# Kernel optimization log

Hardware: AMD Instinct MI355X
Metric: run time of the kernel (lower is better)

## Reference

```python
import jax, jax.numpy as jnp
import numpy as np

K = 3            # TAGConv default number of hops
NUM_GRAPHS = 128 # graphs in the batch (for global_add_pool)


def _gcn_norm(src, dst, n):
    # PyG gcn_norm (symmetric, no self-loops): w_e = d[src]^-1/2 * d[dst]^-1/2
    deg = jnp.zeros((n,), jnp.float32).at[dst].add(1.0)
    dinv = jnp.where(deg > 0, jax.lax.rsqrt(deg), 0.0)
    return dinv[src] * dinv[dst]


def _tagconv(x, src, dst, wn, W, b):
    # out = sum_{k=0..K} (norm_adj^k x) @ W[k] + b
    n = x.shape[0]
    h = x
    out = h @ W[0]
    for k in range(1, K + 1):
        h = jax.ops.segment_sum(h[src] * wn[:, None], dst, num_segments=n)
        out = out + h @ W[k]
    return out + b


def setup_inputs() -> dict:
    key = jax.random.key(0)
    ks = jax.random.split(key, 8)
    N, E, D, H = 50000, 800000, 64, 64
    x = jax.random.normal(ks[0], (N, D), jnp.float32)
    edge_index = jax.random.randint(ks[1], (2, E), 0, N, dtype=jnp.int32)
    batch_ids = jnp.sort(jax.random.randint(ks[2], (N,), 0, NUM_GRAPHS, dtype=jnp.int32))
    def glorot(k, sh):
        return jax.random.normal(k, sh, jnp.float32) / np.float32(np.sqrt(sh[-2]))
    W0 = glorot(ks[3], (K + 1, D, H)); b0 = jnp.zeros((H,), jnp.float32)
    W1 = glorot(ks[4], (K + 1, H, H)); b1 = jnp.zeros((H,), jnp.float32)
    alpha0 = jnp.full((1,), 0.25, jnp.float32)  # PReLU default init
    alpha1 = jnp.full((1,), 0.25, jnp.float32)
    Wout = glorot(ks[5], (H, 1)); bout = jnp.zeros((1,), jnp.float32)
    return dict(x=x, edge_index=edge_index, batch_ids=batch_ids,
                W0=W0, b0=b0, W1=W1, b1=b1,
                alpha0=alpha0, alpha1=alpha1, Wout=Wout, bout=bout)


def reference(x, edge_index, batch_ids, W0, b0, W1, b1, alpha0, alpha1, Wout, bout):
    src, dst = edge_index[0], edge_index[1]
    wn = _gcn_norm(src, dst, x.shape[0])
    # layer 0: TAGConv -> (dropout=identity in eval) -> PReLU
    h = _tagconv(x, src, dst, wn, W0, b0)
    h = jnp.where(h >= 0, h, alpha0 * h)
    # layer 1
    h = _tagconv(h, src, dst, wn, W1, b1)
    h = jnp.where(h >= 0, h, alpha1 * h)
    # global_add_pool over graphs, then linear critic head
    g = jax.ops.segment_sum(h, batch_ids, num_segments=NUM_GRAPHS)  # [G, H]
    return g @ Wout + bout  # [G, 1]
```

## Files before the change

kernel.cpp:

```cpp
#include <hip/hip_runtime.h>
#include <hip/hip_bf16.h>
#include <hip/hip_fp16.h>

#define D 64
#define GRAPHS 128

using bf16x8 = __attribute__((ext_vector_type(8))) short;
using f32x4  = __attribute__((ext_vector_type(4))) float;


__device__ __forceinline__ float bf2f(unsigned short u) {
    return __uint_as_float(((unsigned)u) << 16);
}
__device__ __forceinline__ unsigned short f2bf(float f) {
    unsigned u = __float_as_uint(f);
    unsigned r = (u + 0x7FFFu + ((u >> 16) & 1u)) >> 16;
    return (unsigned short)r;
}


__global__ void deg_prep_kernel(const int* __restrict__ dst, int* __restrict__ deg,
                                int* __restrict__ pos, int E, int EB,
                                const float* __restrict__ W0, const float* __restrict__ W1,
                                unsigned short* __restrict__ WF0, unsigned short* __restrict__ WF1,
                                const float* __restrict__ x, unsigned short* __restrict__ H, int total) {
    int b = blockIdx.x;
    if (b < EB) {
        int e = b * 256 + threadIdx.x;
        if (e < E) pos[e] = atomicAdd(&deg[dst[e]], 1);
    } else if (b < EB + 128) {
        int idx = (b - EB) * 256 + threadIdx.x;
        int i = idx & 16383;
        int j = i & 7, lane = (i >> 3) & 63, ct = (i >> 9) & 3, kt = i >> 11;
        int n = ct * 16 + (lane & 15);
        int k = kt * 32 + (lane >> 4) * 8 + j;
        if (idx < 16384) WF0[i] = f2bf(W0[k * 64 + n]);
        else             WF1[i] = f2bf(W1[k * 64 + n]);
    } else {
        int i = (b - EB - 128) * 256 + threadIdx.x;
        if (i < total) {
            int n = i >> 6, f = i & 63;
            H[(size_t)n * 256 + f] = f2bf(x[i]);
        }
    }
}


__global__ void scan_all_kernel(const int* __restrict__ deg, float* __restrict__ dinv,
                                int* __restrict__ pdeg, int* __restrict__ rowstart,
                                unsigned int* __restrict__ ep, int* __restrict__ total, int N) {
    __shared__ int s[256];
    __shared__ int base_sh;
    int i = blockIdx.x * 256 + threadIdx.x;
    int d = 0, p = 0;
    if (i < N) {
        d = deg[i];
        dinv[i] = d > 0 ? rsqrtf((float)d) : 0.0f;
        p = (d + 7) & ~7;
        pdeg[i] = p;
    }
    s[threadIdx.x] = p;
    __syncthreads();
    for (int st = 1; st < 256; st <<= 1) {
        int add = (threadIdx.x >= st) ? s[threadIdx.x - st] : 0;
        __syncthreads();
        s[threadIdx.x] += add;
        __syncthreads();
    }
    if (threadIdx.x == 255) base_sh = atomicAdd(total, s[255]);
    __syncthreads();
    if (i < N) {
        int excl = base_sh + s[threadIdx.x] - p;
        rowstart[i] = excl;
        for (int q = excl + d; q < excl + p; ++q) ep[q] = 0u;
    }
}


__global__ void scatter_kernel(const int* __restrict__ src, const int* __restrict__ dst,
                               const int* __restrict__ pos, const float* __restrict__ dinv,
                               const int* __restrict__ rowstart, unsigned int* __restrict__ ep, int E) {
    int e = blockIdx.x * blockDim.x + threadIdx.x;
    if (e < E) {
        int d = dst[e], s = src[e];
        unsigned short wu = __half_as_ushort(__float2half(dinv[s]));
        ep[rowstart[d] + pos[e]] = (unsigned)s | ((unsigned)wu << 16);
    }
}


#define GROWS 8

__global__ __launch_bounds__(512, 8)
void gather_kernel(const unsigned short* __restrict__ in,
                   unsigned short* __restrict__ out,
                   const int* __restrict__ rowstart, const int* __restrict__ pdeg,
                   const float* __restrict__ dinv, const unsigned int* __restrict__ ep, int N) {
    int wid = blockIdx.x * GROWS + (threadIdx.x >> 6);
    if (wid >= N) return;
    int lane = threadIdx.x & 63;
    int g  = lane >> 4;
    int fl = (lane & 15) * 4;

    int start = __builtin_amdgcn_readfirstlane(rowstart[wid]);
    int cnt   = __builtin_amdgcn_readfirstlane(pdeg[wid]);
    float dd  = dinv[wid];

    float a0 = 0.f, a1 = 0.f, a2 = 0.f, a3 = 0.f;
    float b0 = 0.f, b1 = 0.f, b2 = 0.f, b3 = 0.f;
    unsigned eA = 0, eB = 0;
    if (cnt > 0) { eA = ep[start + g]; eB = ep[start + 4 + g]; }
    for (int i = 0; i < cnt; i += 8) {
        unsigned cA = eA, cB = eB;
        if (i + 8 < cnt) { eA = ep[start + i + 8 + g]; eB = ep[start + i + 12 + g]; }
        ushort4 rA = *(const ushort4*)(in + (size_t)(cA & 0xFFFFu) * 256 + fl);
        ushort4 rB = *(const ushort4*)(in + (size_t)(cB & 0xFFFFu) * 256 + fl);
        float wA = __half2float(__ushort_as_half((unsigned short)(cA >> 16)));
        float wB = __half2float(__ushort_as_half((unsigned short)(cB >> 16)));
        a0 = fmaf(wA, bf2f(rA.x), a0);
        a1 = fmaf(wA, bf2f(rA.y), a1);
        a2 = fmaf(wA, bf2f(rA.z), a2);
        a3 = fmaf(wA, bf2f(rA.w), a3);
        b0 = fmaf(wB, bf2f(rB.x), b0);
        b1 = fmaf(wB, bf2f(rB.y), b1);
        b2 = fmaf(wB, bf2f(rB.z), b2);
        b3 = fmaf(wB, bf2f(rB.w), b3);
    }
    a0 += b0; a1 += b1; a2 += b2; a3 += b3;
    a0 += __shfl_xor(a0, 16, 64); a0 += __shfl_xor(a0, 32, 64);
    a1 += __shfl_xor(a1, 16, 64); a1 += __shfl_xor(a1, 32, 64);
    a2 += __shfl_xor(a2, 16, 64); a2 += __shfl_xor(a2, 32, 64);
    a3 += __shfl_xor(a3, 16, 64); a3 += __shfl_xor(a3, 32, 64);
    if (g == 0) {
        ushort4 pk;
        pk.x = f2bf(a0 * dd); pk.y = f2bf(a1 * dd); pk.z = f2bf(a2 * dd); pk.w = f2bf(a3 * dd);
        *(ushort4*)(out + (size_t)wid * 256 + fl) = pk;
    }
}


template<int MODE>
__global__ __launch_bounds__(256, 4)
void tag_gemm_kernel(const unsigned short* __restrict__ H,
                     const unsigned short* __restrict__ Wfrag,
                     const float* __restrict__ bias, const float* __restrict__ alpha,
                     const float* __restrict__ Wout, const int* __restrict__ batch,
                     const float* __restrict__ bout,
                     unsigned short* __restrict__ H2, float* __restrict__ outp, int N) {
    __shared__ float bins[GRAPHS];
    if (MODE == 3) {
        if (threadIdx.x < GRAPHS) bins[threadIdx.x] = 0.0f;
        __syncthreads();
    }
    if (MODE == 2) {
        if (blockIdx.x == 0 && threadIdx.x < GRAPHS) outp[threadIdx.x] = bout[0];
    }

    int w = threadIdx.x >> 6, lane = threadIdx.x & 63;
    int m = lane & 15, quad = lane >> 4;
    int rowbase = blockIdx.x * 64 + w * 16;
    int arow = rowbase + m;
    size_t aoff = (size_t)min(arow, N - 1) * 256 + quad * 8;

    f32x4 acc0 = {0.f, 0.f, 0.f, 0.f}, acc1 = acc0, acc2 = acc0, acc3 = acc0;
#pragma unroll
    for (int kt = 0; kt < 8; ++kt) {
        bf16x8 A = *(const bf16x8*)(H + aoff + kt * 32);
        const unsigned short* wf = Wfrag + ((size_t)(kt * 4) * 64 + lane) * 8;
        bf16x8 B0 = *(const bf16x8*)(wf + 0 * 64 * 8);
        bf16x8 B1 = *(const bf16x8*)(wf + 1 * 64 * 8);
        bf16x8 B2 = *(const bf16x8*)(wf + 2 * 64 * 8);
        bf16x8 B3 = *(const bf16x8*)(wf + 3 * 64 * 8);
        acc0 = __builtin_amdgcn_mfma_f32_16x16x32_bf16(A, B0, acc0, 0, 0, 0);
        acc1 = __builtin_amdgcn_mfma_f32_16x16x32_bf16(A, B1, acc1, 0, 0, 0);
        acc2 = __builtin_amdgcn_mfma_f32_16x16x32_bf16(A, B2, acc2, 0, 0, 0);
        acc3 = __builtin_amdgcn_mfma_f32_16x16x32_bf16(A, B3, acc3, 0, 0, 0);
    }

    float al = alpha[0];
    f32x4 accs[4] = {acc0, acc1, acc2, acc3};
    if (MODE == 2) {
#pragma unroll
        for (int ct = 0; ct < 4; ++ct) {
            int col = ct * 16 + m;
            float b = bias[col];
#pragma unroll
            for (int r = 0; r < 4; ++r) {
                int row = rowbase + quad * 4 + r;
                if (row < N) {
                    float v = accs[ct][r] + b;
                    v = v >= 0.f ? v : al * v;
                    H2[(size_t)row * 256 + col] = f2bf(v);
                }
            }
        }
    } else {
        float rv0 = 0.f, rv1 = 0.f, rv2 = 0.f, rv3 = 0.f;
#pragma unroll
        for (int ct = 0; ct < 4; ++ct) {
            int col = ct * 16 + m;
            float b = bias[col], wo = Wout[col];
            float v;
            v = accs[ct][0] + b; v = v >= 0.f ? v : al * v; rv0 = fmaf(v, wo, rv0);
            v = accs[ct][1] + b; v = v >= 0.f ? v : al * v; rv1 = fmaf(v, wo, rv1);
            v = accs[ct][2] + b; v = v >= 0.f ? v : al * v; rv2 = fmaf(v, wo, rv2);
            v = accs[ct][3] + b; v = v >= 0.f ? v : al * v; rv3 = fmaf(v, wo, rv3);
        }
        float rv[4] = {rv0, rv1, rv2, rv3};
#pragma unroll
        for (int r = 0; r < 4; ++r) {
            float v = rv[r];
            v += __shfl_xor(v, 8, 16);
            v += __shfl_xor(v, 4, 16);
            v += __shfl_xor(v, 2, 16);
            v += __shfl_xor(v, 1, 16);
            int row = rowbase + quad * 4 + r;
            if (m == 0 && row < N) atomicAdd(&bins[batch[row]], v);
        }
        __syncthreads();
        if (threadIdx.x < GRAPHS) {
            float bv = bins[threadIdx.x];
            if (bv != 0.0f) atomicAdd(&outp[threadIdx.x], bv);
        }
    }
}

extern "C" void kernel_launch(void* const* d_in, const int* in_sizes, int n_in,
                              void* d_out, int out_size, void* d_ws, size_t ws_size,
                              hipStream_t stream) {
    const float* x     = (const float*)d_in[0];
    const int*   ei    = (const int*)d_in[1];
    const int*   batch = (const int*)d_in[2];
    const float* W0    = (const float*)d_in[3];
    const float* b0    = (const float*)d_in[4];
    const float* W1    = (const float*)d_in[5];
    const float* b1    = (const float*)d_in[6];
    const float* a0    = (const float*)d_in[7];
    const float* a1    = (const float*)d_in[8];
    const float* Wout  = (const float*)d_in[9];
    const float* bout  = (const float*)d_in[10];

    const int N = in_sizes[0] / D;
    const int E = in_sizes[1] / 2;
    const int* src = ei;
    const int* dst = ei + E;

    size_t off = 0;
    auto alloc = [&](size_t bytes) -> void* {
        void* p = (char*)d_ws + off;
        off = (off + bytes + 255) & ~(size_t)255;
        return p;
    };
    const int NB = (N + 255) / 256;
    int*   deg      = (int*)alloc((size_t)(N + 1) * 4);
    int*   pdeg     = (int*)alloc((size_t)N * 4);
    int*   rowstart = (int*)alloc((size_t)N * 4);
    float* dinv     = (float*)alloc((size_t)N * 4);
    int*   pos      = (int*)alloc((size_t)E * 4);
    unsigned int* epack = (unsigned int*)alloc(((size_t)E + 8ull * N) * 4);
    unsigned short* HA = (unsigned short*)alloc((size_t)N * 256 * 2);
    unsigned short* HB = (unsigned short*)alloc((size_t)N * 256 * 2);
    unsigned short* WF0 = (unsigned short*)alloc(16384 * 2);
    unsigned short* WF1 = (unsigned short*)alloc(16384 * 2);

    const int EB = (E + 255) / 256;
    const int NT = (N * D + 255) / 256;
    const int NG = (N + GROWS - 1) / GROWS;
    const int NM = (N + 63) / 64;

    hipMemsetAsync(deg, 0, (size_t)(N + 1) * 4, stream);
    deg_prep_kernel<<<EB + 128 + NT, 256, 0, stream>>>(dst, deg, pos, E, EB,
                                                       W0, W1, WF0, WF1, x, HA, N * D);
    scan_all_kernel<<<NB, 256, 0, stream>>>(deg, dinv, pdeg, rowstart, epack, deg + N, N);
    scatter_kernel<<<EB, 256, 0, stream>>>(src, dst, pos, dinv, rowstart, epack, E);

    gather_kernel<<<NG, 512, 0, stream>>>(HA + 0 * 64, HA + 1 * 64, rowstart, pdeg, dinv, epack, N);
    gather_kernel<<<NG, 512, 0, stream>>>(HA + 1 * 64, HA + 2 * 64, rowstart, pdeg, dinv, epack, N);
    gather_kernel<<<NG, 512, 0, stream>>>(HA + 2 * 64, HA + 3 * 64, rowstart, pdeg, dinv, epack, N);
    tag_gemm_kernel<2><<<NM, 256, 0, stream>>>(HA, WF0, b0, a0, nullptr, nullptr, bout,
                                               HB, (float*)d_out, N);

    gather_kernel<<<NG, 512, 0, stream>>>(HB + 0 * 64, HB + 1 * 64, rowstart, pdeg, dinv, epack, N);
    gather_kernel<<<NG, 512, 0, stream>>>(HB + 1 * 64, HB + 2 * 64, rowstart, pdeg, dinv, epack, N);
    gather_kernel<<<NG, 512, 0, stream>>>(HB + 2 * 64, HB + 3 * 64, rowstart, pdeg, dinv, epack, N);
    tag_gemm_kernel<3><<<NM, 256, 0, stream>>>(HB, WF1, b1, a1, Wout, batch, bout,
                                               nullptr, (float*)d_out, N);
}
```

Baseline: 283.0 us.

## Split feature matrix into 32-wide column panels and gather per panel

Feature storage changes from one 256-wide row per node to panels, each holding 32 features for every node. Each gather launch now covers the two feature halves as separate block ranges, with lanes loading 4-byte pairs, so the neighbour rows touched in one half-pass occupy a smaller footprint that fits the L2/MALL better. The edge-list loads and output stores become nontemporal, and the fused degree/prep kernel is split in two. The cost is reading the edge list twice per hop and issuing narrower, less efficient loads.

Result: slower. 387.5 us (+36.9%).

```diff
diff --git a/kernel.cpp b/kernel.cpp
--- a/kernel.cpp
+++ b/kernel.cpp
@@ -19,17 +19,20 @@
 }
 
 
-__global__ void deg_prep_kernel(const int* __restrict__ dst, int* __restrict__ deg,
-                                int* __restrict__ pos, int E, int EB,
-                                const float* __restrict__ W0, const float* __restrict__ W1,
-                                unsigned short* __restrict__ WF0, unsigned short* __restrict__ WF1,
-                                const float* __restrict__ x, unsigned short* __restrict__ H, int total) {
+__global__ void deg_kernel(const int* __restrict__ dst, int* __restrict__ deg,
+                           int* __restrict__ pos, int E) {
+    int e = blockIdx.x * blockDim.x + threadIdx.x;
+    if (e < E) pos[e] = atomicAdd(&deg[dst[e]], 1);
+}
+
+
+__global__ void prep_kernel(const float* __restrict__ W0, const float* __restrict__ W1,
+                            unsigned short* __restrict__ WF0, unsigned short* __restrict__ WF1,
+                            const float* __restrict__ x, unsigned short* __restrict__ H,
+                            int N, int total) {
     int b = blockIdx.x;
-    if (b < EB) {
-        int e = b * 256 + threadIdx.x;
-        if (e < E) pos[e] = atomicAdd(&deg[dst[e]], 1);
-    } else if (b < EB + 128) {
-        int idx = (b - EB) * 256 + threadIdx.x;
+    if (b < 128) {
+        int idx = b * 256 + threadIdx.x;
         int i = idx & 16383;
         int j = i & 7, lane = (i >> 3) & 63, ct = (i >> 9) & 3, kt = i >> 11;
         int n = ct * 16 + (lane & 15);
@@ -37,10 +40,11 @@
         if (idx < 16384) WF0[i] = f2bf(W0[k * 64 + n]);
         else             WF1[i] = f2bf(W1[k * 64 + n]);
     } else {
-        int i = (b - EB - 128) * 256 + threadIdx.x;
+        int i = (b - 128) * 256 + threadIdx.x;
         if (i < total) {
             int n = i >> 6, f = i & 63;
-            H[(size_t)n * 256 + f] = f2bf(x[i]);
+            int p = f >> 5, fp = f & 31;
+            H[((size_t)(p * 4 + 0) * N + n) * 32 + fp] = f2bf(x[i]);
         }
     }
 }
@@ -92,49 +96,53 @@
 #define GROWS 8
 
 __global__ __launch_bounds__(512, 8)
-void gather_kernel(const unsigned short* __restrict__ in,
-                   unsigned short* __restrict__ out,
+void gather_kernel(const unsigned short* __restrict__ H, int s_in, int s_out,
                    const int* __restrict__ rowstart, const int* __restrict__ pdeg,
-                   const float* __restrict__ dinv, const unsigned int* __restrict__ ep, int N) {
-    int wid = blockIdx.x * GROWS + (threadIdx.x >> 6);
+                   const float* __restrict__ dinv, const unsigned int* __restrict__ ep,
+                   unsigned short* __restrict__ Hout, int N, int NG) {
+    int pb = blockIdx.x;
+    int phase = (pb >= NG) ? 1 : 0;
+    int blk = phase ? pb - NG : pb;
+    int wid = blk * GROWS + (threadIdx.x >> 6);
     if (wid >= N) return;
     int lane = threadIdx.x & 63;
-    int g  = lane >> 4;
-    int fl = (lane & 15) * 4;
+    int g = lane >> 4;
+    int u = lane & 15;
+
+    const unsigned short* in = H    + (size_t)(phase * 4 + s_in)  * N * 32;
+    unsigned short*      out = Hout + (size_t)(phase * 4 + s_out) * N * 32;
 
     int start = __builtin_amdgcn_readfirstlane(rowstart[wid]);
     int cnt   = __builtin_amdgcn_readfirstlane(pdeg[wid]);
     float dd  = dinv[wid];
 
-    float a0 = 0.f, a1 = 0.f, a2 = 0.f, a3 = 0.f;
-    float b0 = 0.f, b1 = 0.f, b2 = 0.f, b3 = 0.f;
+    float a0 = 0.f, a1 = 0.f, b0 = 0.f, b1 = 0.f;
     unsigned eA = 0, eB = 0;
-    if (cnt > 0) { eA = ep[start + g]; eB = ep[start + 4 + g]; }
+    if (cnt > 0) {
+        eA = __builtin_nontemporal_load(&ep[start + g]);
+        eB = __builtin_nontemporal_load(&ep[start + 4 + g]);
+    }
     for (int i = 0; i < cnt; i += 8) {
         unsigned cA = eA, cB = eB;
-        if (i + 8 < cnt) { eA = ep[start + i + 8 + g]; eB = ep[start + i + 12 + g]; }
-        ushort4 rA = *(const ushort4*)(in + (size_t)(cA & 0xFFFFu) * 256 + fl);
-        ushort4 rB = *(const ushort4*)(in + (size_t)(cB & 0xFFFFu) * 256 + fl);
+        if (i + 8 < cnt) {
+            eA = __builtin_nontemporal_load(&ep[start + i + 8 + g]);
+            eB = __builtin_nontemporal_load(&ep[start + i + 12 + g]);
+        }
+        unsigned rA = *(const unsigned*)(in + (size_t)(cA & 0xFFFFu) * 32 + u * 2);
+        unsigned rB = *(const unsigned*)(in + (size_t)(cB & 0xFFFFu) * 32 + u * 2);
         float wA = __half2float(__ushort_as_half((unsigned short)(cA >> 16)));
         float wB = __half2float(__ushort_as_half((unsigned short)(cB >> 16)));
-        a0 = fmaf(wA, bf2f(rA.x), a0);
-        a1 = fmaf(wA, bf2f(rA.y), a1);
-        a2 = fmaf(wA, bf2f(rA.z), a2);
-        a3 = fmaf(wA, bf2f(rA.w), a3);
-        b0 = fmaf(wB, bf2f(rB.x), b0);
-        b1 = fmaf(wB, bf2f(rB.y), b1);
-        b2 = fmaf(wB, bf2f(rB.z), b2);
-        b3 = fmaf(wB, bf2f(rB.w), b3);
-    }
-    a0 += b0; a1 += b1; a2 += b2; a3 += b3;
+        a0 = fmaf(wA, bf2f((unsigned short)rA), a0);
+        a1 = fmaf(wA, bf2f((unsigned short)(rA >> 16)), a1);
+        b0 = fmaf(wB, bf2f((unsigned short)rB), b0);
+        b1 = fmaf(wB, bf2f((unsigned short)(rB >> 16)), b1);
+    }
+    a0 += b0; a1 += b1;
     a0 += __shfl_xor(a0, 16, 64); a0 += __shfl_xor(a0, 32, 64);
     a1 += __shfl_xor(a1, 16, 64); a1 += __shfl_xor(a1, 32, 64);
-    a2 += __shfl_xor(a2, 16, 64); a2 += __shfl_xor(a2, 32, 64);
-    a3 += __shfl_xor(a3, 16, 64); a3 += __shfl_xor(a3, 32, 64);
     if (g == 0) {
-        ushort4 pk;
-        pk.x = f2bf(a0 * dd); pk.y = f2bf(a1 * dd); pk.z = f2bf(a2 * dd); pk.w = f2bf(a3 * dd);
-        *(ushort4*)(out + (size_t)wid * 256 + fl) = pk;
+        unsigned pk = (unsigned)f2bf(a0 * dd) | ((unsigned)f2bf(a1 * dd) << 16);
+        __builtin_nontemporal_store(pk, (unsigned*)(out + (size_t)wid * 32 + u * 2));
     }
 }
 
@@ -159,13 +167,13 @@
     int w = threadIdx.x >> 6, lane = threadIdx.x & 63;
     int m = lane & 15, quad = lane >> 4;
     int rowbase = blockIdx.x * 64 + w * 16;
-    int arow = rowbase + m;
-    size_t aoff = (size_t)min(arow, N - 1) * 256 + quad * 8;
+    int arow = min(rowbase + m, N - 1);
 
     f32x4 acc0 = {0.f, 0.f, 0.f, 0.f}, acc1 = acc0, acc2 = acc0, acc3 = acc0;
 #pragma unroll
     for (int kt = 0; kt < 8; ++kt) {
-        bf16x8 A = *(const bf16x8*)(H + aoff + kt * 32);
+        int p = kt & 1, s = kt >> 1;
+        bf16x8 A = *(const bf16x8*)(H + ((size_t)(p * 4 + s) * N + arow) * 32 + quad * 8);
         const unsigned short* wf = Wfrag + ((size_t)(kt * 4) * 64 + lane) * 8;
         bf16x8 B0 = *(const bf16x8*)(wf + 0 * 64 * 8);
         bf16x8 B1 = *(const bf16x8*)(wf + 1 * 64 * 8);
@@ -183,6 +191,7 @@
 #pragma unroll
         for (int ct = 0; ct < 4; ++ct) {
             int col = ct * 16 + m;
+            int p = col >> 5, fp = col & 31;
             float b = bias[col];
 #pragma unroll
             for (int r = 0; r < 4; ++r) {
@@ -190,7 +199,7 @@
                 if (row < N) {
                     float v = accs[ct][r] + b;
                     v = v >= 0.f ? v : al * v;
-                    H2[(size_t)row * 256 + col] = f2bf(v);
+                    H2[((size_t)(p * 4 + 0) * N + row) * 32 + fp] = f2bf(v);
                 }
             }
         }
@@ -269,20 +278,20 @@
     const int NM = (N + 63) / 64;
 
     hipMemsetAsync(deg, 0, (size_t)(N + 1) * 4, stream);
-    deg_prep_kernel<<<EB + 128 + NT, 256, 0, stream>>>(dst, deg, pos, E, EB,
-                                                       W0, W1, WF0, WF1, x, HA, N * D);
+    deg_kernel<<<EB, 256, 0, stream>>>(dst, deg, pos, E);
+    prep_kernel<<<128 + NT, 256, 0, stream>>>(W0, W1, WF0, WF1, x, HA, N, N * D);
     scan_all_kernel<<<NB, 256, 0, stream>>>(deg, dinv, pdeg, rowstart, epack, deg + N, N);
     scatter_kernel<<<EB, 256, 0, stream>>>(src, dst, pos, dinv, rowstart, epack, E);
 
-    gather_kernel<<<NG, 512, 0, stream>>>(HA + 0 * 64, HA + 1 * 64, rowstart, pdeg, dinv, epack, N);
-    gather_kernel<<<NG, 512, 0, stream>>>(HA + 1 * 64, HA + 2 * 64, rowstart, pdeg, dinv, epack, N);
-    gather_kernel<<<NG, 512, 0, stream>>>(HA + 2 * 64, HA + 3 * 64, rowstart, pdeg, dinv, epack, N);
+    gather_kernel<<<2 * NG, 512, 0, stream>>>(HA, 0, 1, rowstart, pdeg, dinv, epack, HA, N, NG);
+    gather_kernel<<<2 * NG, 512, 0, stream>>>(HA, 1, 2, rowstart, pdeg, dinv, epack, HA, N, NG);
+    gather_kernel<<<2 * NG, 512, 0, stream>>>(HA, 2, 3, rowstart, pdeg, dinv, epack, HA, N, NG);
     tag_gemm_kernel<2><<<NM, 256, 0, stream>>>(HA, WF0, b0, a0, nullptr, nullptr, bout,
                                                HB, (float*)d_out, N);
 
-    gather_kernel<<<NG, 512, 0, stream>>>(HB + 0 * 64, HB + 1 * 64, rowstart, pdeg, dinv, epack, N);
-    gather_kernel<<<NG, 512, 0, stream>>>(HB + 1 * 64, HB + 2 * 64, rowstart, pdeg, dinv, epack, N);
-    gather_kernel<<<NG, 512, 0, stream>>>(HB + 2 * 64, HB + 3 * 64, rowstart, pdeg, dinv, epack, N);
+    gather_kernel<<<2 * NG, 512, 0, stream>>>(HB, 0, 1, rowstart, pdeg, dinv, epack, HB, N, NG);
+    gather_kernel<<<2 * NG, 512, 0, stream>>>(HB, 1, 2, rowstart, pdeg, dinv, epack, HB, N, NG);
+    gather_kernel<<<2 * NG, 512, 0, stream>>>(HB, 2, 3, rowstart, pdeg, dinv, epack, HB, N, NG);
     tag_gemm_kernel<3><<<NM, 256, 0, stream>>>(HB, WF1, b1, a1, Wout, batch, bout,
                                                nullptr, (float*)d_out, N);
 }
```
